# Optimization experiments

Hardware: AMD Instinct MI355X
Metric: run time of the kernel (lower is better)

## Reference

```python
import jax, jax.numpy as jnp
import numpy as np

VOCAB = 50000
EMBED = 512
COMP = 300
B, L = 2048, 200
CENTER = jnp.array([40.7127, -74.0059], dtype=jnp.float32)


def setup_inputs() -> dict:
    key = jax.random.key(0)
    ks = jax.random.split(key, 8)
    words = jax.random.randint(ks[0], (B, L), 0, VOCAB, dtype=jnp.int64)
    features = jax.random.normal(ks[1], (B, 2), dtype=jnp.float32)
    mask = jnp.ones((B, L), dtype=jnp.float32)
    # nn.Linear(vocab_size, embedding_dim): weight [out, in]
    lim1 = 1.0 / np.sqrt(VOCAB)
    W_hidden = jax.random.uniform(ks[2], (EMBED, VOCAB), jnp.float32, -lim1, lim1)
    b_hidden = jax.random.uniform(ks[3], (EMBED,), jnp.float32, -lim1, lim1)
    lim2 = 1.0 / np.sqrt(EMBED)
    W_pi = jax.random.uniform(ks[4], (COMP, EMBED), jnp.float32, -lim2, lim2)
    b_pi = jax.random.uniform(ks[5], (COMP,), jnp.float32, -lim2, lim2)
    # mu = (rand-0.5)*4 + CENTER ; sigma = rand * log(0.01)
    mu = (jax.random.uniform(ks[6], (COMP, 2), jnp.float32) - 0.5) * 4.0 + CENTER
    sigma = jax.random.uniform(ks[7], (COMP, 2), jnp.float32) * np.log(0.01).astype(np.float32)
    return {"words": words, "features": features, "mask": mask,
            "W_hidden": W_hidden, "b_hidden": b_hidden,
            "W_pi": W_pi, "b_pi": b_pi, "mu": mu, "sigma": sigma}


def reference(words, features, mask, W_hidden, b_hidden, W_pi, b_pi, mu, sigma):
    bsz = words.shape[0]
    # binary bag-of-words one-hot: s[words[i]] = 1 (duplicates collapse to 1)
    q = jnp.zeros((bsz, VOCAB), dtype=W_hidden.dtype)
    q = q.at[jnp.arange(bsz)[:, None], words].set(1.0)
    hidden = jnp.tanh(q @ W_hidden.T + b_hidden)          # [B, E]
    pi = jax.nn.softmax(hidden @ W_pi.T + b_pi, axis=-1).T  # [C, B]
    sigma_out = jnp.exp(sigma)                             # [C, 2]
    return pi, sigma_out, mu
```

## Files before the change

kernel.cpp:

```cpp
#include <hip/hip_runtime.h>
#include <cstdint>
#include <cstddef>

#define VOCAB 50000
#define EMBED 512
#define COMP  300
#define LW    200
#define LPAD  208
#define NCHUNK 8
#define CHUNK_ROWS 50048
#define CHUNK_BYTES ((size_t)CHUNK_ROWS * 64)
#define CPAD  320
#define NPART 40

#define QINVSCALE 28398.0633f
#define QSCALE    3.52136689e-05f

__global__ __launch_bounds__(256) void quant_chunk_kernel(
    const float* __restrict__ in, unsigned char* __restrict__ out)
{
    __shared__ float tile[64 * 68];
    const int wBase = blockIdx.x * 64;
    const int c = blockIdx.y;
    const int eBase = c * 64;
    const int t = threadIdx.x;

    {
        const int col4 = t & 15;
        const int w = wBase + col4 * 4;
#pragma unroll
        for (int rr = 0; rr < 4; ++rr) {
            const int el = (t >> 4) + rr * 16;
            float4 v = make_float4(0.f, 0.f, 0.f, 0.f);
            if (w + 3 < VOCAB) {
                v = *(const float4*)&in[(size_t)(eBase + el) * VOCAB + w];
            } else {
                const float* row = &in[(size_t)(eBase + el) * VOCAB];
                v.x = (w + 0 < VOCAB) ? row[w + 0] : 0.f;
                v.y = (w + 1 < VOCAB) ? row[w + 1] : 0.f;
                v.z = (w + 2 < VOCAB) ? row[w + 2] : 0.f;
                v.w = (w + 3 < VOCAB) ? row[w + 3] : 0.f;
            }
            *(float4*)&tile[el * 68 + col4 * 4] = v;
        }
    }
    __syncthreads();

    {
        const int wl = t >> 2;
        const int g = t & 3;
        unsigned int pk[4];
#pragma unroll
        for (int q4 = 0; q4 < 4; ++q4) {
            unsigned int p = 0;
#pragma unroll
            for (int k = 0; k < 4; ++k) {
                const float f = tile[(g * 16 + q4 * 4 + k) * 68 + wl];
                int q = __float2int_rn(f * QINVSCALE) + 128;
                q = q < 0 ? 0 : (q > 255 ? 255 : q);
                p |= (unsigned int)q << (8 * k);
            }
            pk[q4] = p;
        }
        uint4 v = make_uint4(pk[0], pk[1], pk[2], pk[3]);
        *(uint4*)(out + (size_t)c * CHUNK_BYTES + (size_t)(wBase + wl) * 64 + g * 16) = v;
    }
}

__global__ __launch_bounds__(256) void wpi_tail_kernel(
    const float* __restrict__ W_pi, const float* __restrict__ mu,
    const float* __restrict__ sigma, float* __restrict__ Wtp,
    float* __restrict__ out_tail)
{
    __shared__ float tile[32 * 33];
    const int kBase = blockIdx.x * 32;
    const int cBase = blockIdx.y * 32;
    const int t = threadIdx.x;

    {
        const int cr = t >> 3;
        const int k4 = t & 7;
        float4 v = make_float4(0.f, 0.f, 0.f, 0.f);
        if (cBase + cr < COMP)
            v = *(const float4*)&W_pi[(size_t)(cBase + cr) * EMBED + kBase + k4 * 4];
        tile[cr * 33 + k4 * 4 + 0] = v.x;
        tile[cr * 33 + k4 * 4 + 1] = v.y;
        tile[cr * 33 + k4 * 4 + 2] = v.z;
        tile[cr * 33 + k4 * 4 + 3] = v.w;
    }
    __syncthreads();
    {
        const int kr = t >> 3;
        const int c4 = t & 7;
        float4 v;
        v.x = tile[(c4 * 4 + 0) * 33 + kr];
        v.y = tile[(c4 * 4 + 1) * 33 + kr];
        v.z = tile[(c4 * 4 + 2) * 33 + kr];
        v.w = tile[(c4 * 4 + 3) * 33 + kr];
        *(float4*)&Wtp[(size_t)(kBase + kr) * CPAD + cBase + c4 * 4] = v;
    }
    if (blockIdx.x == 0 && blockIdx.y == 0) {
        for (int tt = t; tt < 2 * COMP; tt += 256) {
            out_tail[tt]            = expf(sigma[tt]);
            out_tail[2 * COMP + tt] = mu[tt];
        }
    }
}

__global__ __launch_bounds__(256) void dedup_kernel(
    const int* __restrict__ words, int* __restrict__ soff)
{
    __shared__ int sw[LW];
    const int i = blockIdx.x;
    const int t = threadIdx.x;
    if (t < LW) sw[t] = words[(size_t)i * LW + t];
    __syncthreads();
    if (t < LPAD) {
        int off = VOCAB * 64;
        if (t < LW) {
            const int w = sw[t];
            int dup = 0;
            for (int j = 0; j < t; ++j) dup |= (sw[j] == w);
            off = (dup ? VOCAB : w) * 64;
        }
        soff[(size_t)i * LPAD + t] = off;
    }
}

__global__ __launch_bounds__(256) void gather_kernel(
    const int* __restrict__ soff, const unsigned char* __restrict__ W8,
    const float* __restrict__ b_hidden, float* __restrict__ h)
{
    __shared__ int sOff[LPAD];
    __shared__ float part[256];
    const int b = blockIdx.x;
    const int c = b & 7;
    const int i = b >> 3;
    const int t = threadIdx.x;
    const int w4 = t >> 6, lane = t & 63;

    if (t < LPAD) sOff[t] = soff[(size_t)i * LPAD + t];
    __syncthreads();

    const unsigned char* base = W8 + (size_t)c * CHUNK_BYTES + (lane & 15) * 4;
    const int j = lane >> 4;
    const int l0 = w4 * 52;
    float a0 = 0.f, a1 = 0.f, a2 = 0.f, a3 = 0.f;
#pragma unroll
    for (int s = 0; s < 13; ++s) {
        const int off = sOff[l0 + s * 4 + j];
        const unsigned int d = *(const unsigned int*)(base + (unsigned int)off);
        a0 += (float)(d & 0xffu);
        a1 += (float)((d >> 8) & 0xffu);
        a2 += (float)((d >> 16) & 0xffu);
        a3 += (float)(d >> 24);
    }
    a0 += __shfl_xor(a0, 16); a0 += __shfl_xor(a0, 32);
    a1 += __shfl_xor(a1, 16); a1 += __shfl_xor(a1, 32);
    a2 += __shfl_xor(a2, 16); a2 += __shfl_xor(a2, 32);
    a3 += __shfl_xor(a3, 16); a3 += __shfl_xor(a3, 32);
    if (lane < 16)
        *(float4*)&part[w4 * 64 + lane * 4] = make_float4(a0, a1, a2, a3);
    __syncthreads();

    if (t < 64) {
        const float S = part[t] + part[64 + t] + part[128 + t] + part[192 + t];
        const int e = c * 64 + t;
        h[(size_t)i * EMBED + e] = tanhf((S - 26624.0f) * QSCALE + b_hidden[e]);
    }
}

__global__ __launch_bounds__(256) void htrans_kernel(
    const float* __restrict__ h, float* __restrict__ hT, int B)
{
    __shared__ float tile[64 * 65];
    const int i0 = blockIdx.x * 64;
    const int k0 = blockIdx.y * 64;
    const int t = threadIdx.x;
    const int col4 = t & 15;
    const int row = t >> 4;

#pragma unroll
    for (int rr = 0; rr < 4; ++rr) {
        const int r = row + rr * 16;
        const float4 v = *(const float4*)&h[(size_t)(i0 + r) * EMBED + k0 + col4 * 4];
        tile[r * 65 + col4 * 4 + 0] = v.x;
        tile[r * 65 + col4 * 4 + 1] = v.y;
        tile[r * 65 + col4 * 4 + 2] = v.z;
        tile[r * 65 + col4 * 4 + 3] = v.w;
    }
    __syncthreads();
#pragma unroll
    for (int rr = 0; rr < 4; ++rr) {
        const int kr = row + rr * 16;
        float4 v;
        v.x = tile[(col4 * 4 + 0) * 65 + kr];
        v.y = tile[(col4 * 4 + 1) * 65 + kr];
        v.z = tile[(col4 * 4 + 2) * 65 + kr];
        v.w = tile[(col4 * 4 + 3) * 65 + kr];
        *(float4*)&hT[(size_t)(k0 + kr) * B + i0 + col4 * 4] = v;
    }
}

__global__ __launch_bounds__(256) void logits_kernel(
    const float* __restrict__ hT, const float* __restrict__ Wtp,
    const float* __restrict__ b_pi, float* __restrict__ logit,
    float* __restrict__ pm, float* __restrict__ pl, int B)
{
    __shared__ float sh[128 * 64];
    const int i0 = blockIdx.x * 64;
    const int cblk = blockIdx.y;
    const int t = threadIdx.x;
    const int wv = __builtin_amdgcn_readfirstlane(t >> 6);
    const int lane = t & 63;
    const int c0 = cblk * 32 + wv * 8;

    float acc[8] = {0.f, 0.f, 0.f, 0.f, 0.f, 0.f, 0.f, 0.f};

    for (int ks = 0; ks < EMBED; ks += 128) {
        __syncthreads();
#pragma unroll
        for (int p = 0; p < 8; ++p) {
            const int q = p * 256 + t;
            const int k = q >> 4;
            const int f4 = q & 15;
            *(float4*)&sh[k * 64 + f4 * 4] =
                *(const float4*)&hT[(size_t)(ks + k) * B + i0 + f4 * 4];
        }
        __syncthreads();

#pragma unroll 4
        for (int k = 0; k < 128; ++k) {
            const float hh = sh[k * 64 + lane];
            const float* __restrict__ wrow = &Wtp[(size_t)(ks + k) * CPAD + c0];
#pragma unroll
            for (int jj = 0; jj < 8; ++jj)
                acc[jj] = fmaf(hh, wrow[jj], acc[jj]);
        }
    }

    float vals[8];
    float m = -INFINITY;
#pragma unroll
    for (int jj = 0; jj < 8; ++jj) {
        const int cc = c0 + jj;
        if (cc < COMP) {
            const float v = acc[jj] + b_pi[cc];
            vals[jj] = v;
            logit[(size_t)cc * B + i0 + lane] = v;
            m = fmaxf(m, v);
        } else {
            vals[jj] = -INFINITY;
        }
    }
    float l = 0.f;
#pragma unroll
    for (int jj = 0; jj < 8; ++jj) {
        if (c0 + jj < COMP) l += __expf(vals[jj] - m);
    }
    const int g = cblk * 4 + wv;
    pm[(size_t)g * B + i0 + lane] = m;
    pl[(size_t)g * B + i0 + lane] = l;
}

__global__ __launch_bounds__(64) void softmax_kernel(
    const float* __restrict__ logit, const float* __restrict__ pm,
    const float* __restrict__ pl, float* __restrict__ pi_out, int B)
{
    const int i = blockIdx.x * 64 + threadIdx.x;
    const int part = blockIdx.y;
    float M = -INFINITY;
#pragma unroll 8
    for (int g = 0; g < NPART; ++g) M = fmaxf(M, pm[(size_t)g * B + i]);
    float L = 0.f;
#pragma unroll 8
    for (int g = 0; g < NPART; ++g)
        L += pl[(size_t)g * B + i] * __expf(pm[(size_t)g * B + i] - M);
    const float inv = 1.0f / L;
    const int cEnd = part * 75 + 75;
#pragma unroll 5
    for (int c = part * 75; c < cEnd; ++c) {
        const float x = logit[(size_t)c * B + i];
        pi_out[(size_t)c * B + i] = __expf(x - M) * inv;
    }
}

extern "C" void kernel_launch(void* const* d_in, const int* in_sizes, int n_in,
                              void* d_out, int out_size, void* d_ws, size_t ws_size,
                              hipStream_t stream) {
    const int*   words    = (const int*)d_in[0];
    const float* W_hidden = (const float*)d_in[3];
    const float* b_hidden = (const float*)d_in[4];
    const float* W_pi     = (const float*)d_in[5];
    const float* b_pi     = (const float*)d_in[6];
    const float* mu       = (const float*)d_in[7];
    const float* sigma    = (const float*)d_in[8];
    float* out = (float*)d_out;

    const int B = in_sizes[0] / LW;

    unsigned char* W8   = (unsigned char*)d_ws;
    int*   soff  = (int*)(W8 + NCHUNK * CHUNK_BYTES);
    float* h     = (float*)(soff + (size_t)B * LPAD);
    float* hT    = h  + (size_t)B * EMBED;
    float* Wtp   = hT + (size_t)EMBED * B;
    float* logit = Wtp + (size_t)EMBED * CPAD;
    float* pm    = logit + (size_t)COMP * B;
    float* pl    = pm + (size_t)NPART * B;

    hipLaunchKernelGGL(quant_chunk_kernel, dim3(CHUNK_ROWS / 64, NCHUNK), dim3(256),
                       0, stream, W_hidden, W8);
    hipLaunchKernelGGL(wpi_tail_kernel, dim3(EMBED / 32, CPAD / 32), dim3(256),
                       0, stream, W_pi, mu, sigma, Wtp, out + (size_t)COMP * B);
    hipLaunchKernelGGL(dedup_kernel, dim3(B), dim3(256), 0, stream, words, soff);
    hipLaunchKernelGGL(gather_kernel, dim3(B * NCHUNK), dim3(256), 0, stream,
                       soff, W8, b_hidden, h);
    hipLaunchKernelGGL(htrans_kernel, dim3(B / 64, EMBED / 64), dim3(256),
                       0, stream, h, hT, B);
    hipLaunchKernelGGL(logits_kernel, dim3(B / 64, 10), dim3(256), 0, stream,
                       hT, Wtp, b_pi, logit, pm, pl, B);
    hipLaunchKernelGGL(softmax_kernel, dim3(B / 64, 4), dim3(64), 0, stream,
                       logit, pm, pl, out, B);
}
```

Measured before the change: 262.0 us.

## Batch gather rows, retile logits with LDS weights, swizzle quant tile

Several kernels change at once. The quant kernel swaps its grid order so the chunk index varies fastest, applies an XOR-like swizzle to the LDS tile to avoid bank conflicts, and drops the per-element tail handling. The gather kernel now handles four batch rows per block, which gives more loads in flight per thread. The logits kernel stages a 16-column slice of W_pi in LDS, works on 128 samples per block and doubles the number of softmax partials. The risks are more LDS and register pressure, and the simplified tail load in the quant kernel, which assumes VOCAB is a multiple of 4.

```diff
diff --git a/kernel.cpp b/kernel.cpp
--- a/kernel.cpp
+++ b/kernel.cpp
@@ -11,7 +11,7 @@
 #define CHUNK_ROWS 50048
 #define CHUNK_BYTES ((size_t)CHUNK_ROWS * 64)
 #define CPAD  320
-#define NPART 40
+#define NPART 80
 
 #define QINVSCALE 28398.0633f
 #define QSCALE    3.52136689e-05f
@@ -20,9 +20,9 @@
     const float* __restrict__ in, unsigned char* __restrict__ out)
 {
     __shared__ float tile[64 * 68];
-    const int wBase = blockIdx.x * 64;
-    const int c = blockIdx.y;
-    const int eBase = c * 64;
+    const int cc = blockIdx.x;
+    const int wBase = blockIdx.y * 64;
+    const int eBase = cc * 64;
     const int t = threadIdx.x;
 
     {
@@ -32,16 +32,10 @@
         for (int rr = 0; rr < 4; ++rr) {
             const int el = (t >> 4) + rr * 16;
             float4 v = make_float4(0.f, 0.f, 0.f, 0.f);
-            if (w + 3 < VOCAB) {
+            if (w < VOCAB)
                 v = *(const float4*)&in[(size_t)(eBase + el) * VOCAB + w];
-            } else {
-                const float* row = &in[(size_t)(eBase + el) * VOCAB];
-                v.x = (w + 0 < VOCAB) ? row[w + 0] : 0.f;
-                v.y = (w + 1 < VOCAB) ? row[w + 1] : 0.f;
-                v.z = (w + 2 < VOCAB) ? row[w + 2] : 0.f;
-                v.w = (w + 3 < VOCAB) ? row[w + 3] : 0.f;
-            }
-            *(float4*)&tile[el * 68 + col4 * 4] = v;
+            const int sw = (col4 * 4 + 8 * ((el >> 4) & 3)) & 63;
+            *(float4*)&tile[el * 68 + sw] = v;
         }
     }
     __syncthreads();
@@ -55,7 +49,8 @@
             unsigned int p = 0;
 #pragma unroll
             for (int k = 0; k < 4; ++k) {
-                const float f = tile[(g * 16 + q4 * 4 + k) * 68 + wl];
+                const int e = g * 16 + q4 * 4 + k;
+                const float f = tile[e * 68 + ((wl + 8 * g) & 63)];
                 int q = __float2int_rn(f * QINVSCALE) + 128;
                 q = q < 0 ? 0 : (q > 255 ? 255 : q);
                 p |= (unsigned int)q << (8 * k);
@@ -63,7 +58,7 @@
             pk[q4] = p;
         }
         uint4 v = make_uint4(pk[0], pk[1], pk[2], pk[3]);
-        *(uint4*)(out + (size_t)c * CHUNK_BYTES + (size_t)(wBase + wl) * 64 + g * 16) = v;
+        *(uint4*)(out + (size_t)cc * CHUNK_BYTES + (size_t)(wBase + wl) * 64 + g * 16) = v;
     }
 }
 
@@ -131,42 +126,61 @@
     const int* __restrict__ soff, const unsigned char* __restrict__ W8,
     const float* __restrict__ b_hidden, float* __restrict__ h)
 {
-    __shared__ int sOff[LPAD];
-    __shared__ float part[256];
+    __shared__ int sOff[4 * LPAD];
+    __shared__ float part[4][256];
     const int b = blockIdx.x;
     const int c = b & 7;
-    const int i = b >> 3;
+    const int ip = b >> 3;
+    const int i0 = ip * 4;
     const int t = threadIdx.x;
     const int w4 = t >> 6, lane = t & 63;
 
-    if (t < LPAD) sOff[t] = soff[(size_t)i * LPAD + t];
+    if (t < LPAD) {
+#pragma unroll
+        for (int r = 0; r < 4; ++r)
+            sOff[r * LPAD + t] = soff[(size_t)(i0 + r) * LPAD + t];
+    }
     __syncthreads();
 
     const unsigned char* base = W8 + (size_t)c * CHUNK_BYTES + (lane & 15) * 4;
     const int j = lane >> 4;
     const int l0 = w4 * 52;
-    float a0 = 0.f, a1 = 0.f, a2 = 0.f, a3 = 0.f;
+    float ac[4][4];
+#pragma unroll
+    for (int r = 0; r < 4; ++r)
+#pragma unroll
+        for (int q = 0; q < 4; ++q) ac[r][q] = 0.f;
+
 #pragma unroll
     for (int s = 0; s < 13; ++s) {
-        const int off = sOff[l0 + s * 4 + j];
-        const unsigned int d = *(const unsigned int*)(base + (unsigned int)off);
-        a0 += (float)(d & 0xffu);
-        a1 += (float)((d >> 8) & 0xffu);
-        a2 += (float)((d >> 16) & 0xffu);
-        a3 += (float)(d >> 24);
-    }
-    a0 += __shfl_xor(a0, 16); a0 += __shfl_xor(a0, 32);
-    a1 += __shfl_xor(a1, 16); a1 += __shfl_xor(a1, 32);
-    a2 += __shfl_xor(a2, 16); a2 += __shfl_xor(a2, 32);
-    a3 += __shfl_xor(a3, 16); a3 += __shfl_xor(a3, 32);
-    if (lane < 16)
-        *(float4*)&part[w4 * 64 + lane * 4] = make_float4(a0, a1, a2, a3);
-    __syncthreads();
-
-    if (t < 64) {
-        const float S = part[t] + part[64 + t] + part[128 + t] + part[192 + t];
-        const int e = c * 64 + t;
-        h[(size_t)i * EMBED + e] = tanhf((S - 26624.0f) * QSCALE + b_hidden[e]);
+#pragma unroll
+        for (int r = 0; r < 4; ++r) {
+            const int off = sOff[r * LPAD + l0 + s * 4 + j];
+            const unsigned int d = *(const unsigned int*)(base + (unsigned int)off);
+            ac[r][0] += (float)(d & 0xffu);
+            ac[r][1] += (float)((d >> 8) & 0xffu);
+            ac[r][2] += (float)((d >> 16) & 0xffu);
+            ac[r][3] += (float)(d >> 24);
+        }
+    }
+#pragma unroll
+    for (int r = 0; r < 4; ++r) {
+#pragma unroll
+        for (int q = 0; q < 4; ++q) {
+            ac[r][q] += __shfl_xor(ac[r][q], 16);
+            ac[r][q] += __shfl_xor(ac[r][q], 32);
+        }
+        if (lane < 16)
+            *(float4*)&part[r][w4 * 64 + lane * 4] =
+                make_float4(ac[r][0], ac[r][1], ac[r][2], ac[r][3]);
+    }
+    __syncthreads();
+
+    {
+        const int r = w4, d = lane;
+        const float S = part[r][d] + part[r][64 + d] + part[r][128 + d] + part[r][192 + d];
+        const int e = c * 64 + d;
+        h[(size_t)(i0 + r) * EMBED + e] = tanhf((S - 26624.0f) * QSCALE + b_hidden[e]);
     }
 }
 
@@ -207,60 +221,82 @@
     const float* __restrict__ b_pi, float* __restrict__ logit,
     float* __restrict__ pm, float* __restrict__ pl, int B)
 {
-    __shared__ float sh[128 * 64];
-    const int i0 = blockIdx.x * 64;
+    __shared__ float wt[512 * 16];
+    __shared__ float sh[64 * 128];
+    const int i0 = blockIdx.x * 128;
     const int cblk = blockIdx.y;
+    const int c0base = cblk * 16;
     const int t = threadIdx.x;
     const int wv = __builtin_amdgcn_readfirstlane(t >> 6);
     const int lane = t & 63;
-    const int c0 = cblk * 32 + wv * 8;
+
+#pragma unroll
+    for (int p = 0; p < 8; ++p) {
+        const int q = p * 256 + t;
+        const int k = q >> 2;
+        const int c4 = q & 3;
+        *(float4*)&wt[k * 16 + c4 * 4] =
+            *(const float4*)&Wtp[(size_t)k * CPAD + c0base + c4 * 4];
+    }
 
     float acc[8] = {0.f, 0.f, 0.f, 0.f, 0.f, 0.f, 0.f, 0.f};
 
-    for (int ks = 0; ks < EMBED; ks += 128) {
+    for (int ks = 0; ks < EMBED; ks += 64) {
         __syncthreads();
 #pragma unroll
         for (int p = 0; p < 8; ++p) {
             const int q = p * 256 + t;
-            const int k = q >> 4;
-            const int f4 = q & 15;
-            *(float4*)&sh[k * 64 + f4 * 4] =
+            const int k = q >> 5;
+            const int f4 = q & 31;
+            *(float4*)&sh[k * 128 + f4 * 4] =
                 *(const float4*)&hT[(size_t)(ks + k) * B + i0 + f4 * 4];
         }
         __syncthreads();
 
-#pragma unroll 4
-        for (int k = 0; k < 128; ++k) {
-            const float hh = sh[k * 64 + lane];
-            const float* __restrict__ wrow = &Wtp[(size_t)(ks + k) * CPAD + c0];
-#pragma unroll
-            for (int jj = 0; jj < 8; ++jj)
-                acc[jj] = fmaf(hh, wrow[jj], acc[jj]);
-        }
-    }
-
-    float vals[8];
-    float m = -INFINITY;
-#pragma unroll
-    for (int jj = 0; jj < 8; ++jj) {
-        const int cc = c0 + jj;
+#pragma unroll 8
+        for (int k = 0; k < 64; ++k) {
+            const float4 w = *(const float4*)&wt[(ks + k) * 16 + wv * 4];
+            const float h0 = sh[k * 128 + lane];
+            const float h1 = sh[k * 128 + 64 + lane];
+            acc[0] = fmaf(h0, w.x, acc[0]);
+            acc[1] = fmaf(h0, w.y, acc[1]);
+            acc[2] = fmaf(h0, w.z, acc[2]);
+            acc[3] = fmaf(h0, w.w, acc[3]);
+            acc[4] = fmaf(h1, w.x, acc[4]);
+            acc[5] = fmaf(h1, w.y, acc[5]);
+            acc[6] = fmaf(h1, w.z, acc[6]);
+            acc[7] = fmaf(h1, w.w, acc[7]);
+        }
+    }
+
+    float v0[4], v1[4];
+    float m0 = -INFINITY, m1 = -INFINITY;
+#pragma unroll
+    for (int q = 0; q < 4; ++q) {
+        const int cc = c0base + wv * 4 + q;
+        const float bp = (cc < COMP) ? b_pi[cc] : 0.f;
+        v0[q] = acc[q] + bp;
+        v1[q] = acc[4 + q] + bp;
         if (cc < COMP) {
-            const float v = acc[jj] + b_pi[cc];
-            vals[jj] = v;
-            logit[(size_t)cc * B + i0 + lane] = v;
-            m = fmaxf(m, v);
-        } else {
-            vals[jj] = -INFINITY;
-        }
-    }
-    float l = 0.f;
-#pragma unroll
-    for (int jj = 0; jj < 8; ++jj) {
-        if (c0 + jj < COMP) l += __expf(vals[jj] - m);
+            logit[(size_t)cc * B + i0 + lane] = v0[q];
+            logit[(size_t)cc * B + i0 + 64 + lane] = v1[q];
+            m0 = fmaxf(m0, v0[q]);
+            m1 = fmaxf(m1, v1[q]);
+        }
+    }
+    float l0 = 0.f, l1 = 0.f;
+#pragma unroll
+    for (int q = 0; q < 4; ++q) {
+        if (c0base + wv * 4 + q < COMP) {
+            l0 += __expf(v0[q] - m0);
+            l1 += __expf(v1[q] - m1);
+        }
     }
     const int g = cblk * 4 + wv;
-    pm[(size_t)g * B + i0 + lane] = m;
-    pl[(size_t)g * B + i0 + lane] = l;
+    pm[(size_t)g * B + i0 + lane] = m0;
+    pl[(size_t)g * B + i0 + lane] = l0;
+    pm[(size_t)g * B + i0 + 64 + lane] = m1;
+    pl[(size_t)g * B + i0 + 64 + lane] = l1;
 }
 
 __global__ __launch_bounds__(64) void softmax_kernel(
@@ -308,16 +344,16 @@
     float* pm    = logit + (size_t)COMP * B;
     float* pl    = pm + (size_t)NPART * B;
 
-    hipLaunchKernelGGL(quant_chunk_kernel, dim3(CHUNK_ROWS / 64, NCHUNK), dim3(256),
+    hipLaunchKernelGGL(quant_chunk_kernel, dim3(NCHUNK, CHUNK_ROWS / 64), dim3(256),
                        0, stream, W_hidden, W8);
     hipLaunchKernelGGL(wpi_tail_kernel, dim3(EMBED / 32, CPAD / 32), dim3(256),
                        0, stream, W_pi, mu, sigma, Wtp, out + (size_t)COMP * B);
     hipLaunchKernelGGL(dedup_kernel, dim3(B), dim3(256), 0, stream, words, soff);
-    hipLaunchKernelGGL(gather_kernel, dim3(B * NCHUNK), dim3(256), 0, stream,
+    hipLaunchKernelGGL(gather_kernel, dim3((B / 4) * NCHUNK), dim3(256), 0, stream,
                        soff, W8, b_hidden, h);
     hipLaunchKernelGGL(htrans_kernel, dim3(B / 64, EMBED / 64), dim3(256),
                        0, stream, h, hT, B);
-    hipLaunchKernelGGL(logits_kernel, dim3(B / 64, 10), dim3(256), 0, stream,
+    hipLaunchKernelGGL(logits_kernel, dim3(B / 128, 20), dim3(256), 0, stream,
                        hT, Wtp, b_pi, logit, pm, pl, B);
     hipLaunchKernelGGL(softmax_kernel, dim3(B / 64, 4), dim3(64), 0, stream,
                        logit, pm, pl, out, B);
```

Result: faster. 254.8 us (-2.7%).
